# Kernel tuning notes

Hardware: AMD Instinct MI355X
Metric: run time of the kernel (lower is better)

The kernel has to match this reference:

```python
import jax, jax.numpy as jnp
import numpy as np

D_EMB = 1024
D_ATTN = 1024
NUM_HEADS = 16
HEAD_DIM = D_ATTN // NUM_HEADS
SEQ = 2048
BS = 2


def setup_inputs() -> dict:
    key = jax.random.key(0)
    ks = jax.random.split(key, 6)
    s = 1.0 / np.sqrt(D_EMB)
    return {
        "x": jax.random.normal(ks[0], (BS, SEQ, D_EMB), dtype=jnp.float32),
        "W_q": jax.random.uniform(ks[1], (D_ATTN, D_EMB), jnp.float32, -s, s),
        "W_k": jax.random.uniform(ks[2], (D_ATTN, D_EMB), jnp.float32, -s, s),
        "W_v": jax.random.uniform(ks[3], (D_ATTN, D_EMB), jnp.float32, -s, s),
        "W_o": jax.random.uniform(ks[4], (D_ATTN, D_ATTN), jnp.float32, -s, s),
        "b_o": jax.random.uniform(ks[5], (D_ATTN,), jnp.float32, -s, s),
    }


def reference(x, W_q, W_k, W_v, W_o, b_o):
    bs, seq_len, _ = x.shape
    # QKV projections (torch Linear: x @ W.T)
    q = jnp.einsum('bse,ae->bsa', x, W_q).reshape(bs, seq_len, NUM_HEADS, HEAD_DIM)
    k = jnp.einsum('bse,ae->bsa', x, W_k).reshape(bs, seq_len, NUM_HEADS, HEAD_DIM)
    v = jnp.einsum('bse,ae->bsa', x, W_v).reshape(bs, seq_len, NUM_HEADS, HEAD_DIM)
    # [b, h, s, d]
    q = q.transpose(0, 2, 1, 3)
    k = k.transpose(0, 2, 1, 3)
    v = v.transpose(0, 2, 1, 3)
    # scores [b, h, s, s] with causal mask
    scores = jnp.einsum('bhqd,bhkd->bhqk', q, k)
    causal = jnp.tril(jnp.ones((seq_len, seq_len), dtype=bool))
    scores = jnp.where(causal, scores, -jnp.inf)
    attn = jax.nn.softmax(scores / np.sqrt(HEAD_DIM), axis=-1)
    # dropout p=0.0 -> identity
    ctx = jnp.einsum('bhqk,bhkd->bhqd', attn, v)
    ctx = ctx.transpose(0, 2, 1, 3).reshape(bs, seq_len, D_ATTN)
    return jnp.einsum('bsa,oa->bso', ctx, W_o) + b_o
```

## Files before the change

### kernel.cpp

```cpp
#include <hip/hip_runtime.h>
#include <stdint.h>

#define SEQ   2048
#define DEMB  1024
#define NH    16
#define HD    64
#define MROWS 4096

typedef __bf16 bf16x8 __attribute__((ext_vector_type(8)));
typedef __bf16 bf16x4 __attribute__((ext_vector_type(4)));
typedef float  f32x4  __attribute__((ext_vector_type(4)));

#define MFMA(a, b, c) __builtin_amdgcn_mfma_f32_16x16x32_bf16((a), (b), (c), 0, 0, 0)

static __device__ __forceinline__ uint16_t f2bf(float f) {
  union { __bf16 b; uint16_t u; } c;
  c.b = (__bf16)f;
  return c.u;
}

static __device__ __forceinline__ ushort4 pack4(f32x4 f) {
  union { bf16x4 b; ushort4 u; } c;
  c.b[0] = (__bf16)f[0]; c.b[1] = (__bf16)f[1];
  c.b[2] = (__bf16)f[2]; c.b[3] = (__bf16)f[3];
  return c.u;
}

static __device__ __forceinline__ bf16x8 ldb8(const uint16_t* p) {
  union { uint4 i; bf16x8 b; } u;
  u.i = *(const uint4*)p;
  return u.b;
}

static __device__ __forceinline__ void gld_lds16(const uint16_t* g, uint16_t* l) {
  __builtin_amdgcn_global_load_lds(
      (const __attribute__((address_space(1))) uint32_t*)(g),
      (__attribute__((address_space(3))) uint32_t*)(l),
      16, 0, 0);
}

__global__ __launch_bounds__(256) void cvt_all(const float* __restrict__ x,
                                               const float* __restrict__ wq,
                                               const float* __restrict__ wk,
                                               const float* __restrict__ wv,
                                               const float* __restrict__ wo,
                                               uint16_t* __restrict__ xb,
                                               uint16_t* __restrict__ wqkv,
                                               uint16_t* __restrict__ wob) {
  const int bid = blockIdx.x;
  const float* src; uint16_t* dst; int off;
  if (bid < 4096)      { src = x;  dst = xb;                 off = bid; }
  else if (bid < 5120) { src = wq; dst = wqkv;               off = bid - 4096; }
  else if (bid < 6144) { src = wk; dst = wqkv + (1u << 20);  off = bid - 5120; }
  else if (bid < 7168) { src = wv; dst = wqkv + (2u << 20);  off = bid - 6144; }
  else                 { src = wo; dst = wob;                off = bid - 7168; }
  const int i = (off * 256 + threadIdx.x) * 4;
  float4 v = *(const float4*)(src + i);
  f32x4 f; f[0] = v.x; f[1] = v.y; f[2] = v.z; f[3] = v.w;
  *(ushort4*)(dst + i) = pack4(f);
}

template <int MODE>
__global__ __launch_bounds__(256) void gemm_bt(const uint16_t* __restrict__ A,
                                               const uint16_t* __restrict__ B,
                                               uint16_t* __restrict__ Cq,
                                               uint16_t* __restrict__ Ck,
                                               uint16_t* __restrict__ Cvt,
                                               float* __restrict__ Cf,
                                               const float* __restrict__ bias,
                                               int K) {
  constexpr int BN = (MODE == 2) ? 64 : 128;
  constexpr int NI = (MODE == 2) ? 2 : 4;
  __shared__ uint16_t As[2][128 * 32];
  __shared__ uint16_t Bs[2][BN * 32];
  const int t  = threadIdx.x;
  const int l  = t & 63;
  const int li = l & 15, lg = l >> 4;
  const int w  = t >> 6;
  const int wr = (w >> 1) << 6;
  const int wc = (MODE == 2) ? ((w & 1) << 5) : ((w & 1) << 6);
  const int brow = blockIdx.y << 7;
  const int bcol = blockIdx.x * BN;

  const uint16_t* ga0 = A + (size_t)(brow + (t >> 2)) * K + (t & 3) * 8;
  const uint16_t* ga1 = ga0 + (size_t)64 * K;
  const uint16_t* gb0 = B + (size_t)(bcol + (t >> 2)) * K + (t & 3) * 8;
  const uint16_t* gb1 = gb0 + (size_t)64 * K;

  auto stage = [&](int buf, int k0) {
    gld_lds16(ga0 + k0, &As[buf][t * 8]);
    gld_lds16(ga1 + k0, &As[buf][2048 + t * 8]);
    gld_lds16(gb0 + k0, &Bs[buf][t * 8]);
    if (BN == 128) gld_lds16(gb1 + k0, &Bs[buf][2048 + t * 8]);
  };

  f32x4 acc[4][NI] = {};

  stage(0, 0);
  __syncthreads();
  int cur = 0;

  for (int k0 = 0; k0 < K; k0 += 32) {
    if (k0 + 32 < K) stage(cur ^ 1, k0 + 32);

    bf16x8 af[4], bfr[NI];
#pragma unroll
    for (int i = 0; i < 4; ++i)
      af[i] = ldb8(&As[cur][(wr + i * 16 + li) * 32 + lg * 8]);
#pragma unroll
    for (int i = 0; i < NI; ++i)
      bfr[i] = ldb8(&Bs[cur][(wc + i * 16 + li) * 32 + lg * 8]);
#pragma unroll
    for (int mi = 0; mi < 4; ++mi)
#pragma unroll
      for (int ni = 0; ni < NI; ++ni)
        acc[mi][ni] = MFMA(af[mi], bfr[ni], acc[mi][ni]);

    __syncthreads();
    cur ^= 1;
  }

#pragma unroll
  for (int mi = 0; mi < 4; ++mi) {
#pragma unroll
    for (int ni = 0; ni < NI; ++ni) {
      const int row = brow + wr + mi * 16 + lg * 4;
      const int col = bcol + wc + ni * 16 + li;
#pragma unroll
      for (int r = 0; r < 4; ++r) {
        const float v = acc[mi][ni][r];
        if (MODE == 0) {
          if (col < 1024) {
            Cq[(size_t)(row + r) * 1024 + col] = f2bf(v * 0.18033688f);
          } else if (col < 2048) {
            Ck[(size_t)(row + r) * 1024 + (col - 1024)] = f2bf(v);
          } else {
            const int c = col - 2048;
            const int m = row + r;
            Cvt[((size_t)c + (size_t)((m >> 11) << 10)) * 2048 + (m & 2047)] = f2bf(v);
          }
        } else {
          Cf[(size_t)(row + r) * 1024 + col] = v + bias[col];
        }
      }
    }
  }
}

__global__ __launch_bounds__(256) void attn_fwd(const uint16_t* __restrict__ Q,
                                                const uint16_t* __restrict__ K,
                                                const uint16_t* __restrict__ Vt,
                                                uint16_t* __restrict__ ctx) {
  const int bh = blockIdx.x;
  const int qb = 31 - blockIdx.y;
  const int b  = bh >> 4, h = bh & 15;
  const int t  = threadIdx.x;
  const int w  = t >> 6, l = t & 63;
  const int li = l & 15, lg = l >> 4;

  __shared__ uint16_t Kl[2][64 * 64];
  __shared__ uint16_t Vl[2][64 * 64];
  __shared__ uint16_t P[4][16][72];

  const uint16_t* Kg = K + (size_t)(b * 2048) * 1024 + h * 64;
  const uint16_t* Vg = Vt + (size_t)(b * 1024 + h * 64) * 2048;

  const int srow = t >> 3;
  const int scol = ((t & 7) * 8) ^ ((srow & 7) * 8);

  const int qrow = (qb << 6) + (w << 4);
  const uint16_t* qp = Q + (size_t)(b * 2048 + qrow + li) * 1024 + h * 64 + lg * 8;
  const bf16x8 q0 = ldb8(qp);
  const bf16x8 q1 = ldb8(qp + 32);

  f32x4 o[4] = {};
  float m_r = -1e30f, l_r = 0.f;

  auto stage = [&](int buf, int kt2) {
    const int kb2 = kt2 << 6;
    gld_lds16(Kg + (size_t)(kb2 + srow) * 1024 + scol,      &Kl[buf][t * 8]);
    gld_lds16(Kg + (size_t)(kb2 + 32 + srow) * 1024 + scol, &Kl[buf][2048 + t * 8]);
    gld_lds16(Vg + (size_t)srow * 2048 + kb2 + scol,        &Vl[buf][t * 8]);
    gld_lds16(Vg + (size_t)(32 + srow) * 2048 + kb2 + scol, &Vl[buf][2048 + t * 8]);
  };

  stage(0, 0);
  __syncthreads();
  int cur = 0;

  const int fsw = (li & 7) * 8;

  for (int kt = 0; kt <= qb; ++kt) {
    if (kt < qb) stage(cur ^ 1, kt + 1);

    const uint16_t* Kc = &Kl[cur][0];
    const uint16_t* Vc = &Vl[cur][0];

    f32x4 s[4];
#pragma unroll
    for (int tt = 0; tt < 4; ++tt) {
      const uint16_t* kr = Kc + (tt * 16 + li) * 64;
      f32x4 z = {};
      z = MFMA(ldb8(kr + ((lg * 8) ^ fsw)), q0, z);
      z = MFMA(ldb8(kr + ((32 + lg * 8) ^ fsw)), q1, z);
      s[tt] = z;
    }

    bf16x8 vf[4][2];
#pragma unroll
    for (int dt = 0; dt < 4; ++dt) {
      const uint16_t* vr = Vc + (dt * 16 + li) * 64;
      vf[dt][0] = ldb8(vr + ((lg * 8) ^ fsw));
      vf[dt][1] = ldb8(vr + ((32 + lg * 8) ^ fsw));
    }

    if (kt == qb) {
      const int qloc = (w << 4) + li;
#pragma unroll
      for (int tt = 0; tt < 4; ++tt) {
        const int key = (tt << 4) + (lg << 2);
#pragma unroll
        for (int r = 0; r < 4; ++r)
          if (key + r > qloc) s[tt][r] = -1e30f;
      }
    }

    float tm = fmaxf(fmaxf(s[0][0], s[0][1]), fmaxf(s[0][2], s[0][3]));
#pragma unroll
    for (int tt = 1; tt < 4; ++tt)
      tm = fmaxf(tm, fmaxf(fmaxf(s[tt][0], s[tt][1]), fmaxf(s[tt][2], s[tt][3])));
    tm = fmaxf(tm, __shfl_xor(tm, 16));
    tm = fmaxf(tm, __shfl_xor(tm, 32));

    if (!__all(tm - m_r <= 8.f)) {
      const float mn = fmaxf(m_r, tm);
      const float corr = __builtin_amdgcn_exp2f(m_r - mn);
      m_r = mn;
      l_r *= corr;
#pragma unroll
      for (int dt = 0; dt < 4; ++dt) {
        o[dt][0] *= corr; o[dt][1] *= corr; o[dt][2] *= corr; o[dt][3] *= corr;
      }
    }

    float sum = 0.f;
    ushort4 pk[4];
#pragma unroll
    for (int tt = 0; tt < 4; ++tt) {
      f32x4 p;
      p[0] = __builtin_amdgcn_exp2f(s[tt][0] - m_r);
      p[1] = __builtin_amdgcn_exp2f(s[tt][1] - m_r);
      p[2] = __builtin_amdgcn_exp2f(s[tt][2] - m_r);
      p[3] = __builtin_amdgcn_exp2f(s[tt][3] - m_r);
      sum += (p[0] + p[1]) + (p[2] + p[3]);
      pk[tt] = pack4(p);
    }
    sum += __shfl_xor(sum, 16);
    sum += __shfl_xor(sum, 32);
    l_r += sum;

#pragma unroll
    for (int tt = 0; tt < 4; ++tt)
      *(ushort4*)&P[w][li][(tt << 4) + (lg << 2)] = pk[tt];
    asm volatile("s_waitcnt lgkmcnt(0)" ::: "memory");

    const bf16x8 pb0 = ldb8(&P[w][li][lg * 8]);
    const bf16x8 pb1 = ldb8(&P[w][li][32 + lg * 8]);
#pragma unroll
    for (int dt = 0; dt < 4; ++dt) {
      o[dt] = MFMA(vf[dt][0], pb0, o[dt]);
      o[dt] = MFMA(vf[dt][1], pb1, o[dt]);
    }

    __syncthreads();
    cur ^= 1;
  }

  const float inv = 1.0f / l_r;
  const int qg = b * 2048 + qrow + li;
#pragma unroll
  for (int dt = 0; dt < 4; ++dt) {
    f32x4 ov = o[dt];
    ov[0] *= inv; ov[1] *= inv; ov[2] *= inv; ov[3] *= inv;
    *(ushort4*)(ctx + (size_t)qg * 1024 + h * 64 + (dt << 4) + (lg << 2)) = pack4(ov);
  }
}

extern "C" void kernel_launch(void* const* d_in, const int* in_sizes, int n_in,
                              void* d_out, int out_size, void* d_ws, size_t ws_size,
                              hipStream_t stream) {
  const float* x  = (const float*)d_in[0];
  const float* Wq = (const float*)d_in[1];
  const float* Wk = (const float*)d_in[2];
  const float* Wv = (const float*)d_in[3];
  const float* Wo = (const float*)d_in[4];
  const float* bo = (const float*)d_in[5];
  float* out = (float*)d_out;

  char* ws = (char*)d_ws;
  uint16_t* xb   = (uint16_t*)(ws);
  uint16_t* Wqkv = (uint16_t*)(ws + ( 8u << 20));
  uint16_t* Wob  = (uint16_t*)(ws + (14u << 20));
  uint16_t* Qb   = (uint16_t*)(ws + (16u << 20));
  uint16_t* Kb   = (uint16_t*)(ws + (24u << 20));
  uint16_t* Vt   = (uint16_t*)(ws + (32u << 20));
  uint16_t* Ctx  = (uint16_t*)(ws);

  cvt_all<<<8192, 256, 0, stream>>>(x, Wq, Wk, Wv, Wo, xb, Wqkv, Wob);

  gemm_bt<0><<<dim3(24, 32), 256, 0, stream>>>(xb, Wqkv, Qb, Kb, Vt,
                                               nullptr, nullptr, 1024);

  attn_fwd<<<dim3(32, 32), 256, 0, stream>>>(Qb, Kb, Vt, Ctx);

  gemm_bt<2><<<dim3(16, 32), 256, 0, stream>>>(Ctx, Wob, nullptr, nullptr, nullptr,
                                               out, bo, 1024);
}
```

Baseline: 115.4 us.

## Rewrite QKV GEMM with 256x256 tiles, swizzled LDS and interleaved staging

Replaces the templated QKV projection GEMM with a dedicated 512-thread kernel. It uses 256x256 output tiles, a 64-wide K step with XOR-swizzled LDS, and a four-phase loop that interleaves global-to-LDS prefetch with MFMA bursts using s_setprio and explicit waitcnt/barriers. The goal is better operand reuse, fewer LDS bank conflicts and better overlap of memory with compute. The trade-off is only 192 blocks, a large LDS footprint (128 KB per block) and heavy register pressure. It also adds setprio hints around the MFMA sections in the attention kernel and splits the output GEMM into its own kernel.

Result: slower. 152.3 us (+31.9%).

```diff
diff --git a/kernel.cpp b/kernel.cpp
--- a/kernel.cpp
+++ b/kernel.cpp
@@ -60,41 +60,203 @@
   *(ushort4*)(dst + i) = pack4(f);
 }
 
-template <int MODE>
-__global__ __launch_bounds__(256) void gemm_bt(const uint16_t* __restrict__ A,
-                                               const uint16_t* __restrict__ B,
-                                               uint16_t* __restrict__ Cq,
-                                               uint16_t* __restrict__ Ck,
-                                               uint16_t* __restrict__ Cvt,
-                                               float* __restrict__ Cf,
-                                               const float* __restrict__ bias,
-                                               int K) {
-  constexpr int BN = (MODE == 2) ? 64 : 128;
-  constexpr int NI = (MODE == 2) ? 2 : 4;
+__global__ __launch_bounds__(512, 2) void gemm_qkv(const uint16_t* __restrict__ A,
+                                                   const uint16_t* __restrict__ B,
+                                                   uint16_t* __restrict__ Cq,
+                                                   uint16_t* __restrict__ Ck,
+                                                   uint16_t* __restrict__ Cvt) {
+  constexpr int K = 1024;
+  __shared__ uint16_t As[2][256 * 64];
+  __shared__ uint16_t Bs[2][256 * 64];
+  const int t  = threadIdx.x;
+  const int l  = t & 63;
+  const int li = l & 15, lg = l >> 4;
+  const int w  = t >> 6;
+  const int wm = w >> 2, wn = w & 3;
+  const int brow = blockIdx.y << 8, bcol = blockIdx.x << 8;
+
+  const int srow = t >> 3;
+  const int scol = ((t & 7) ^ (srow & 7)) << 3;
+  const uint16_t* gA = A + (size_t)(brow + srow) * K + scol;
+  const uint16_t* gB = B + (size_t)(bcol + srow) * K + scol;
+
+  const int swz = li & 7;
+
+  auto stA = [&](int buf, int k0, int r0) {
+    gld_lds16(gA + (size_t)r0 * K + k0, &As[buf][(r0 << 6) + t * 8]);
+  };
+  auto stB = [&](int buf, int k0, int r0) {
+    gld_lds16(gB + (size_t)r0 * K + k0, &Bs[buf][(r0 << 6) + t * 8]);
+  };
+  auto ldA = [&](int buf, int mh, int kh, int fi) {
+    const int row = wm * 128 + mh * 64 + fi * 16 + li;
+    return ldb8(&As[buf][(row << 6) + ((((kh << 2) + lg) ^ swz) << 3)]);
+  };
+  auto ldB = [&](int buf, int kh, int ni) {
+    const int row = wn * 64 + ni * 16 + li;
+    return ldb8(&Bs[buf][(row << 6) + ((((kh << 2) + lg) ^ swz) << 3)]);
+  };
+
+  f32x4 acc[8][4] = {};
+  bf16x8 af[4], bfr[4];
+
+  stA(0, 0, 0); stA(0, 0, 128);
+  stB(0, 0, 0); stB(0, 0, 64); stB(0, 0, 128); stB(0, 0, 192);
+  stA(0, 0, 64); stA(0, 0, 192);
+  asm volatile("s_waitcnt vmcnt(0)" ::: "memory");
+  __builtin_amdgcn_s_barrier();
+
+  int cur = 0;
+  for (int kt = 0; kt < 15; ++kt) {
+    const int kn = (kt + 1) << 6;
+    const int nb = cur ^ 1;
+
+    stA(nb, kn, 0); stA(nb, kn, 128);
+    __builtin_amdgcn_sched_barrier(0);
+#pragma unroll
+    for (int ni = 0; ni < 4; ++ni) bfr[ni] = ldB(cur, 0, ni);
+#pragma unroll
+    for (int fi = 0; fi < 4; ++fi) af[fi] = ldA(cur, 0, 0, fi);
+    __builtin_amdgcn_s_setprio(1);
+#pragma unroll
+    for (int fi = 0; fi < 4; ++fi)
+#pragma unroll
+      for (int ni = 0; ni < 4; ++ni)
+        acc[fi][ni] = MFMA(af[fi], bfr[ni], acc[fi][ni]);
+    __builtin_amdgcn_s_setprio(0);
+    asm volatile("s_waitcnt vmcnt(2)" ::: "memory");
+    __builtin_amdgcn_s_barrier();
+
+    stB(nb, kn, 0); stB(nb, kn, 64);
+    __builtin_amdgcn_sched_barrier(0);
+#pragma unroll
+    for (int fi = 0; fi < 4; ++fi) af[fi] = ldA(cur, 1, 0, fi);
+    __builtin_amdgcn_s_setprio(1);
+#pragma unroll
+    for (int fi = 0; fi < 4; ++fi)
+#pragma unroll
+      for (int ni = 0; ni < 4; ++ni)
+        acc[4 + fi][ni] = MFMA(af[fi], bfr[ni], acc[4 + fi][ni]);
+    __builtin_amdgcn_s_setprio(0);
+    __builtin_amdgcn_s_barrier();
+
+    stB(nb, kn, 128); stB(nb, kn, 192);
+    __builtin_amdgcn_sched_barrier(0);
+#pragma unroll
+    for (int ni = 0; ni < 4; ++ni) bfr[ni] = ldB(cur, 1, ni);
+#pragma unroll
+    for (int fi = 0; fi < 4; ++fi) af[fi] = ldA(cur, 0, 1, fi);
+    __builtin_amdgcn_s_setprio(1);
+#pragma unroll
+    for (int fi = 0; fi < 4; ++fi)
+#pragma unroll
+      for (int ni = 0; ni < 4; ++ni)
+        acc[fi][ni] = MFMA(af[fi], bfr[ni], acc[fi][ni]);
+    __builtin_amdgcn_s_setprio(0);
+    __builtin_amdgcn_s_barrier();
+
+    stA(nb, kn, 64); stA(nb, kn, 192);
+    __builtin_amdgcn_sched_barrier(0);
+#pragma unroll
+    for (int fi = 0; fi < 4; ++fi) af[fi] = ldA(cur, 1, 1, fi);
+    __builtin_amdgcn_s_setprio(1);
+#pragma unroll
+    for (int fi = 0; fi < 4; ++fi)
+#pragma unroll
+      for (int ni = 0; ni < 4; ++ni)
+        acc[4 + fi][ni] = MFMA(af[fi], bfr[ni], acc[4 + fi][ni]);
+    __builtin_amdgcn_s_setprio(0);
+    asm volatile("s_waitcnt vmcnt(2)" ::: "memory");
+    __builtin_amdgcn_s_barrier();
+
+    cur = nb;
+  }
+
+#pragma unroll
+  for (int ni = 0; ni < 4; ++ni) bfr[ni] = ldB(cur, 0, ni);
+#pragma unroll
+  for (int fi = 0; fi < 4; ++fi) af[fi] = ldA(cur, 0, 0, fi);
+#pragma unroll
+  for (int fi = 0; fi < 4; ++fi)
+#pragma unroll
+    for (int ni = 0; ni < 4; ++ni)
+      acc[fi][ni] = MFMA(af[fi], bfr[ni], acc[fi][ni]);
+  asm volatile("s_waitcnt vmcnt(0)" ::: "memory");
+  __builtin_amdgcn_s_barrier();
+#pragma unroll
+  for (int fi = 0; fi < 4; ++fi) af[fi] = ldA(cur, 1, 0, fi);
+#pragma unroll
+  for (int fi = 0; fi < 4; ++fi)
+#pragma unroll
+    for (int ni = 0; ni < 4; ++ni)
+      acc[4 + fi][ni] = MFMA(af[fi], bfr[ni], acc[4 + fi][ni]);
+#pragma unroll
+  for (int ni = 0; ni < 4; ++ni) bfr[ni] = ldB(cur, 1, ni);
+#pragma unroll
+  for (int fi = 0; fi < 4; ++fi) af[fi] = ldA(cur, 0, 1, fi);
+#pragma unroll
+  for (int fi = 0; fi < 4; ++fi)
+#pragma unroll
+    for (int ni = 0; ni < 4; ++ni)
+      acc[fi][ni] = MFMA(af[fi], bfr[ni], acc[fi][ni]);
+#pragma unroll
+  for (int fi = 0; fi < 4; ++fi) af[fi] = ldA(cur, 1, 1, fi);
+#pragma unroll
+  for (int fi = 0; fi < 4; ++fi)
+#pragma unroll
+    for (int ni = 0; ni < 4; ++ni)
+      acc[4 + fi][ni] = MFMA(af[fi], bfr[ni], acc[4 + fi][ni]);
+
+#pragma unroll
+  for (int mi = 0; mi < 8; ++mi) {
+#pragma unroll
+    for (int ni = 0; ni < 4; ++ni) {
+      const int row = brow + wm * 128 + mi * 16 + lg * 4;
+      const int col = bcol + wn * 64 + ni * 16 + li;
+#pragma unroll
+      for (int r = 0; r < 4; ++r) {
+        const float v = acc[mi][ni][r];
+        if (col < 1024) {
+          Cq[(size_t)(row + r) * 1024 + col] = f2bf(v * 0.18033688f);
+        } else if (col < 2048) {
+          Ck[(size_t)(row + r) * 1024 + (col - 1024)] = f2bf(v);
+        } else {
+          const int c = col - 2048;
+          const int m = row + r;
+          Cvt[((size_t)c + (size_t)((m >> 11) << 10)) * 2048 + (m & 2047)] = f2bf(v);
+        }
+      }
+    }
+  }
+}
+
+__global__ __launch_bounds__(256) void gemm_out(const uint16_t* __restrict__ A,
+                                                const uint16_t* __restrict__ B,
+                                                float* __restrict__ Cf,
+                                                const float* __restrict__ bias) {
+  constexpr int K = 1024;
   __shared__ uint16_t As[2][128 * 32];
-  __shared__ uint16_t Bs[2][BN * 32];
+  __shared__ uint16_t Bs[2][64 * 32];
   const int t  = threadIdx.x;
   const int l  = t & 63;
   const int li = l & 15, lg = l >> 4;
   const int w  = t >> 6;
   const int wr = (w >> 1) << 6;
-  const int wc = (MODE == 2) ? ((w & 1) << 5) : ((w & 1) << 6);
+  const int wc = (w & 1) << 5;
   const int brow = blockIdx.y << 7;
-  const int bcol = blockIdx.x * BN;
+  const int bcol = blockIdx.x << 6;
 
   const uint16_t* ga0 = A + (size_t)(brow + (t >> 2)) * K + (t & 3) * 8;
   const uint16_t* ga1 = ga0 + (size_t)64 * K;
   const uint16_t* gb0 = B + (size_t)(bcol + (t >> 2)) * K + (t & 3) * 8;
-  const uint16_t* gb1 = gb0 + (size_t)64 * K;
 
   auto stage = [&](int buf, int k0) {
     gld_lds16(ga0 + k0, &As[buf][t * 8]);
     gld_lds16(ga1 + k0, &As[buf][2048 + t * 8]);
     gld_lds16(gb0 + k0, &Bs[buf][t * 8]);
-    if (BN == 128) gld_lds16(gb1 + k0, &Bs[buf][2048 + t * 8]);
-  };
-
-  f32x4 acc[4][NI] = {};
+  };
+
+  f32x4 acc[4][2] = {};
 
   stage(0, 0);
   __syncthreads();
@@ -103,17 +265,17 @@
   for (int k0 = 0; k0 < K; k0 += 32) {
     if (k0 + 32 < K) stage(cur ^ 1, k0 + 32);
 
-    bf16x8 af[4], bfr[NI];
+    bf16x8 af[4], bfr[2];
 #pragma unroll
     for (int i = 0; i < 4; ++i)
       af[i] = ldb8(&As[cur][(wr + i * 16 + li) * 32 + lg * 8]);
 #pragma unroll
-    for (int i = 0; i < NI; ++i)
+    for (int i = 0; i < 2; ++i)
       bfr[i] = ldb8(&Bs[cur][(wc + i * 16 + li) * 32 + lg * 8]);
 #pragma unroll
     for (int mi = 0; mi < 4; ++mi)
 #pragma unroll
-      for (int ni = 0; ni < NI; ++ni)
+      for (int ni = 0; ni < 2; ++ni)
         acc[mi][ni] = MFMA(af[mi], bfr[ni], acc[mi][ni]);
 
     __syncthreads();
@@ -123,26 +285,12 @@
 #pragma unroll
   for (int mi = 0; mi < 4; ++mi) {
 #pragma unroll
-    for (int ni = 0; ni < NI; ++ni) {
+    for (int ni = 0; ni < 2; ++ni) {
       const int row = brow + wr + mi * 16 + lg * 4;
       const int col = bcol + wc + ni * 16 + li;
 #pragma unroll
-      for (int r = 0; r < 4; ++r) {
-        const float v = acc[mi][ni][r];
-        if (MODE == 0) {
-          if (col < 1024) {
-            Cq[(size_t)(row + r) * 1024 + col] = f2bf(v * 0.18033688f);
-          } else if (col < 2048) {
-            Ck[(size_t)(row + r) * 1024 + (col - 1024)] = f2bf(v);
-          } else {
-            const int c = col - 2048;
-            const int m = row + r;
-            Cvt[((size_t)c + (size_t)((m >> 11) << 10)) * 2048 + (m & 2047)] = f2bf(v);
-          }
-        } else {
-          Cf[(size_t)(row + r) * 1024 + col] = v + bias[col];
-        }
-      }
+      for (int r = 0; r < 4; ++r)
+        Cf[(size_t)(row + r) * 1024 + col] = acc[mi][ni][r] + bias[col];
     }
   }
 }
@@ -197,6 +345,7 @@
     const uint16_t* Vc = &Vl[cur][0];
 
     f32x4 s[4];
+    __builtin_amdgcn_s_setprio(1);
 #pragma unroll
     for (int tt = 0; tt < 4; ++tt) {
       const uint16_t* kr = Kc + (tt * 16 + li) * 64;
@@ -205,6 +354,7 @@
       z = MFMA(ldb8(kr + ((32 + lg * 8) ^ fsw)), q1, z);
       s[tt] = z;
     }
+    __builtin_amdgcn_s_setprio(0);
 
     bf16x8 vf[4][2];
 #pragma unroll
@@ -266,11 +416,13 @@
 
     const bf16x8 pb0 = ldb8(&P[w][li][lg * 8]);
     const bf16x8 pb1 = ldb8(&P[w][li][32 + lg * 8]);
+    __builtin_amdgcn_s_setprio(1);
 #pragma unroll
     for (int dt = 0; dt < 4; ++dt) {
       o[dt] = MFMA(vf[dt][0], pb0, o[dt]);
       o[dt] = MFMA(vf[dt][1], pb1, o[dt]);
     }
+    __builtin_amdgcn_s_setprio(0);
 
     __syncthreads();
     cur ^= 1;
@@ -308,11 +460,9 @@
 
   cvt_all<<<8192, 256, 0, stream>>>(x, Wq, Wk, Wv, Wo, xb, Wqkv, Wob);
 
-  gemm_bt<0><<<dim3(24, 32), 256, 0, stream>>>(xb, Wqkv, Qb, Kb, Vt,
-                                               nullptr, nullptr, 1024);
+  gemm_qkv<<<dim3(12, 16), 512, 0, stream>>>(xb, Wqkv, Qb, Kb, Vt);
 
   attn_fwd<<<dim3(32, 32), 256, 0, stream>>>(Qb, Kb, Vt, Ctx);
 
-  gemm_bt<2><<<dim3(16, 32), 256, 0, stream>>>(Ctx, Wob, nullptr, nullptr, nullptr,
-                                               out, bo, 1024);
-}
+  gemm_out<<<dim3(16, 32), 256, 0, stream>>>(Ctx, Wob, out, bo);
+}
```
